# Optimization experiments

Measured on AMD Instinct MI355X. Metric: run time of the kernel, lower is better.

Reference implementation:

```python
import jax, jax.numpy as jnp
import numpy as np

C = 64

def setup_inputs() -> dict:
    key = jax.random.key(0)
    k1, k2, k3 = jax.random.split(key, 3)
    x = jax.random.normal(k1, (4, C, 64, 64), dtype=jnp.float32)
    # 1x1 conv weight/bias (kernel dims squeezed)
    W = jax.random.normal(k2, (C, C), dtype=jnp.float32) * (1.0 / np.sqrt(C))
    bconv = jax.random.normal(k3, (C,), dtype=jnp.float32) * 0.01
    return {"x": x, "W": W, "bconv": bconv}

def reference(x, W, bconv):
    b, c, h, w = x.shape
    hw = h * w
    # shared 1x1 conv: e = f = g (module applies the same conv three times)
    e = jnp.einsum('oc,bchw->bohw', W, x) + bconv[None, :, None, None]
    e = e.reshape(b, c, hw)
    # unscaled attention scores: (b, hw, hw)
    scores = jnp.einsum('bci,bcj->bij', e, e)
    attn = jax.nn.softmax(scores, axis=-1)
    # g @ attn: (b, c, hw)
    final = jnp.einsum('bci,bij->bcj', e, attn)
    return final.reshape(b, c, h, w) + x
```

## Files before the change

### kernel.cpp

```cpp
#include <hip/hip_runtime.h>
#include <math.h>

#define B 4
#define C 64
#define HW 4096

typedef _Float16 f16;
typedef f16 f16x8 __attribute__((ext_vector_type(8)));
typedef f16 f16x4 __attribute__((ext_vector_type(4)));
typedef f16 f16x2 __attribute__((ext_vector_type(2)));
typedef float f32x4 __attribute__((ext_vector_type(4)));
typedef float f32x16 __attribute__((ext_vector_type(16)));
typedef int i32x4 __attribute__((ext_vector_type(4)));
typedef f16x8 f16x8a __attribute__((aligned(8)));

#define MFMA16(a,b,c) __builtin_amdgcn_mfma_f32_16x16x32_f16(a,b,c,0,0,0)
#define MFMA32(a,b,c) __builtin_amdgcn_mfma_f32_32x32x16_f16(a,b,c,0,0,0)


__device__ __forceinline__ int swz_blk()     { int r = blockIdx.x; return (r & 7) * 32  + (r >> 3); }
__device__ __forceinline__ int swz_blk512()  { int r = blockIdx.x; return (r & 7) * 64  + (r >> 3); }
__device__ __forceinline__ int swz_blk2048() { int r = blockIdx.x; return (r & 7) * 256 + (r >> 3); }

__global__ __launch_bounds__(256) void k_e(
    const float* __restrict__ x, const float* __restrict__ W,
    const float* __restrict__ bconv, f16* __restrict__ et, f16* __restrict__ ec,
    float* __restrict__ mbuf)
{
  __shared__ float Ws[64][65];
  __shared__ float xs[64][64];
  __shared__ f16 es[64][72];
  __shared__ float msp[4][64];
  const int blk = swz_blk();
  const int b = blk >> 6;
  const int i0 = (blk & 63) * 64;
  const int tid = threadIdx.x;

  for (int k = tid; k < 64 * 64; k += 256) Ws[k >> 6][k & 63] = W[k];
  for (int k = tid; k < 64 * 64; k += 256)
    xs[k >> 6][k & 63] = x[((size_t)b * C + (k >> 6)) * HW + i0 + (k & 63)];
  __syncthreads();

  const int o = tid & 63;
  const int ig = tid >> 6;
  float acc[16];
  float bv = bconv[o];
  #pragma unroll
  for (int k = 0; k < 16; ++k) acc[k] = bv;
  for (int c = 0; c < C; ++c) {
    float wv = Ws[o][c];
    #pragma unroll
    for (int k = 0; k < 16; ++k) acc[k] = fmaf(wv, xs[c][ig * 16 + k], acc[k]);
  }
  #pragma unroll
  for (int k = 0; k < 16; ++k) {
    int ii = ig * 16 + k;
    f16 v = (f16)acc[k];
    et[((size_t)b * HW + i0 + ii) * C + o] = v;
    es[o][ii] = v;
  }
  __syncthreads();

  const int ii = tid & 63, og = tid >> 6;
  #pragma unroll
  for (int k = 0; k < 16; ++k) {
    int oo = og * 16 + k;
    ec[((size_t)b * C + oo) * HW + i0 + ii] = es[oo][ii];
  }

  {
    float s = 0.f;
    #pragma unroll
    for (int k = 0; k < 16; ++k) {
      float v = (float)es[og * 16 + k][ii];
      s = fmaf(v, v, s);
    }
    msp[og][ii] = s;
  }
  __syncthreads();
  if (tid < 64) {
    float mm = msp[0][tid] + msp[1][tid] + msp[2][tid] + msp[3][tid];
    mbuf[(size_t)b * HW + i0 + tid] = (float)(f16)mm;
  }
}

__global__ __launch_bounds__(256) __attribute__((amdgpu_waves_per_eu(4, 4)))
void k_stats(const f16* __restrict__ et, const float* __restrict__ mbuf,
             float* __restrict__ lpartial)
{
  __shared__ float lpart[4][36];
  const int blk = swz_blk2048();
  const int b  = blk >> 9;
  const int ib = (blk >> 2) & 127;
  const int jq = blk & 3;
  const int i0 = ib * 32;
  const int tid = threadIdx.x;
  const int wv = tid >> 6;
  const int lane = tid & 63;
  const int lr = lane & 15, lg = lane >> 4;
  const f16* etb = et + (size_t)b * HW * C;

  f16x8 a[2][2];
  #pragma unroll
  for (int is = 0; is < 2; ++is)
    #pragma unroll
    for (int kc = 0; kc < 2; ++kc)
      a[is][kc] = *(const f16x8*)(etb + (size_t)(i0 + is * 16 + lr) * C + kc * 32 + lg * 8);

  f32x4 ms4[2];
  #pragma unroll
  for (int is = 0; is < 2; ++is)
    ms4[is] = *(const f32x4*)(mbuf + (size_t)b * HW + i0 + is * 16 + lg * 4);

  float lacc[2][4] = {};
  for (int t = 0; t < 8; ++t) {
    const int j0 = jq * 1024 + (wv + 4 * t) * 32;
    #pragma unroll
    for (int js = 0; js < 2; ++js) {
      f16x8 b0 = *(const f16x8*)(etb + (size_t)(j0 + js * 16 + lr) * C + lg * 8);
      f16x8 b1 = *(const f16x8*)(etb + (size_t)(j0 + js * 16 + lr) * C + 32 + lg * 8);
      #pragma unroll
      for (int is = 0; is < 2; ++is) {
        f32x4 z = {0.f, 0.f, 0.f, 0.f};
        f32x4 S = MFMA16(a[is][0], b0, z);
        S = MFMA16(a[is][1], b1, S);
        #pragma unroll
        for (int r = 0; r < 4; ++r) lacc[is][r] += __expf(S[r] - ms4[is][r]);
      }
    }
  }

  #pragma unroll
  for (int m = 1; m < 16; m <<= 1)
    #pragma unroll
    for (int is = 0; is < 2; ++is)
      #pragma unroll
      for (int r = 0; r < 4; ++r) lacc[is][r] += __shfl_xor(lacc[is][r], m);

  if (lr == 0)
    #pragma unroll
    for (int is = 0; is < 2; ++is)
      #pragma unroll
      for (int r = 0; r < 4; ++r) lpart[wv][is * 16 + lg * 4 + r] = lacc[is][r];
  __syncthreads();

  if (tid < 32)
    lpartial[((size_t)b * HW + i0 + tid) * 4 + jq] =
        lpart[0][tid] + lpart[1][tid] + lpart[2][tid] + lpart[3][tid];
}

#define ETS 68
#define ECS 36
__global__ __launch_bounds__(512, 4) void k_out(
    const f16* __restrict__ et, const f16* __restrict__ ec,
    const float* __restrict__ mbuf, const float* __restrict__ lpartial,
    f16* __restrict__ partial)
{
  __shared__ __align__(16) f16 etL[2][32][ETS];
  __shared__ __align__(16) f16 ecL[2][64][ECS];
  __shared__ __align__(16) f16 maugAll[513][8];
  const int blk = swz_blk512();
  const int b  = blk >> 7;
  const int jb = (blk >> 3) & 15;
  const int iq = blk & 7;
  const int tid = threadIdx.x;
  const int w = tid >> 6;
  const int lane = tid & 63;
  const int l31 = lane & 31;
  const int h = lane >> 5;
  const int jbase = jb * 256 + w * 32;
  const int ibase = iq * 512;

  const f16* etb = et + (size_t)b * HW * C;
  const f16* ecb = ec + (size_t)b * C * HW;

  {
    float m = mbuf[(size_t)b * HW + ibase + tid];
    f32x4 lp = *(const f32x4*)&lpartial[((size_t)b * HW + ibase + tid) * 4];
    float l = lp[0] + lp[1] + lp[2] + lp[3];
    float d = __logf(l);
    f16 dh = (f16)d;
    f16 dl = (f16)(d - (float)dh);
    f16x8 row = {};
    row[0] = (f16)m; row[1] = dh; row[2] = dl;
    *(f16x8*)&maugAll[tid][0] = row;
    if (tid == 0) { f16x8 zz = {}; *(f16x8*)&maugAll[512][0] = zz; }
  }

  f16x8 baug = {};
  if (h == 0) { baug[0] = (f16)-1.f; baug[1] = (f16)-1.f; baug[2] = (f16)-1.f; }

  f16x8 bj[4];
  #pragma unroll
  for (int kc = 0; kc < 4; ++kc)
    bj[kc] = *(const f16x8*)(etb + (size_t)(jbase + l31) * C + kc * 16 + h * 8);

  f32x16 acc[2] = {};

  const bool se = (tid < 256);
  const int sei = tid >> 3;
  const int sec = (tid & 7) * 8;
  const int scc = (tid & 255) >> 2;
  const int sci = (tid & 3) * 8;

  if (se) *(f16x8a*)&etL[0][sei][sec] = *(const f16x8*)(etb + (size_t)(ibase + sei) * C + sec);
  else    *(f16x8a*)&ecL[0][scc][sci] = *(const f16x8*)(ecb + (size_t)scc * HW + ibase + sci);
  __syncthreads();

  for (int t = 0; t < 16; ++t) {
    const int cur = t & 1;
    const int i0c = ibase + t * 32;

    f16x8 sv;
    if (t < 15) {
      if (se) sv = *(const f16x8*)(etb + (size_t)(i0c + 32 + sei) * C + sec);
      else    sv = *(const f16x8*)(ecb + (size_t)scc * HW + (i0c + 32) + sci);
    }

    f16x8 bv[2][2];
    #pragma unroll
    for (int cs = 0; cs < 2; ++cs)
      #pragma unroll
      for (int kf = 0; kf < 2; ++kf)
        bv[cs][kf] = *(const f16x8a*)&ecL[cur][cs * 32 + l31][kf * 16 + h * 8];

    f16x8 af[4];
    #pragma unroll
    for (int kc = 0; kc < 4; ++kc)
      af[kc] = *(const f16x8a*)&etL[cur][l31][kc * 16 + h * 8];
    f16x8 aaug = *(const f16x8*)&maugAll[h ? 512 : (t * 32 + l31)][0];

    f32x16 z = {};
    f32x16 S = MFMA32(af[0], bj[0], z);
    S = MFMA32(af[1], bj[1], S);
    S = MFMA32(af[2], bj[2], S);
    S = MFMA32(af[3], bj[3], S);
    S = MFMA32(aaug, baug, S);

    float E[16];
    #pragma unroll
    for (int r = 0; r < 16; ++r) E[r] = __expf(S[r]);

    f16x8 pa[2];
    #pragma unroll
    for (int kf = 0; kf < 2; ++kf) {
      int A0 = __builtin_bit_cast(int, __builtin_amdgcn_cvt_pkrtz(E[kf * 8 + 0], E[kf * 8 + 1]));
      int A1 = __builtin_bit_cast(int, __builtin_amdgcn_cvt_pkrtz(E[kf * 8 + 2], E[kf * 8 + 3]));
      int B0 = __builtin_bit_cast(int, __builtin_amdgcn_cvt_pkrtz(E[kf * 8 + 4], E[kf * 8 + 5]));
      int B1 = __builtin_bit_cast(int, __builtin_amdgcn_cvt_pkrtz(E[kf * 8 + 6], E[kf * 8 + 7]));
      asm volatile("v_permlane32_swap_b32 %0, %1" : "+v"(A0), "+v"(B0));
      asm volatile("v_permlane32_swap_b32 %0, %1" : "+v"(A1), "+v"(B1));
      i32x4 fri = {A0, A1, B0, B1};
      pa[kf] = __builtin_bit_cast(f16x8, fri);
    }

    acc[0] = MFMA32(pa[0], bv[0][0], acc[0]);
    acc[1] = MFMA32(pa[0], bv[1][0], acc[1]);
    acc[0] = MFMA32(pa[1], bv[0][1], acc[0]);
    acc[1] = MFMA32(pa[1], bv[1][1], acc[1]);

    if (t < 15) {
      if (se) *(f16x8a*)&etL[cur ^ 1][sei][sec] = sv;
      else    *(f16x8a*)&ecL[cur ^ 1][scc][sci] = sv;
    }
    __syncthreads();
  }

  f16* pb = partial + (size_t)(iq * B + b) * HW * C;
  #pragma unroll
  for (int cs = 0; cs < 2; ++cs)
    #pragma unroll
    for (int r = 0; r < 16; ++r) {
      int j = jbase + (r & 3) + 8 * (r >> 2) + 4 * h;
      pb[(size_t)j * C + cs * 32 + l31] = (f16)acc[cs][r];
    }
}

__global__ __launch_bounds__(256) void k_reduce(
    const f16* __restrict__ partial, const float* __restrict__ x, float* __restrict__ out)
{
  __shared__ float tile[64][65];
  const int blk = swz_blk();
  const int b = blk >> 6;
  const int j0 = (blk & 63) * 64;
  const int tid = threadIdx.x;
  const int jj = tid >> 2, cq = (tid & 3) * 16;

  float a0[16] = {};
  for (int iq = 0; iq < 8; ++iq) {
    const f16* p = partial + ((size_t)(iq * B + b) * HW + j0 + jj) * C + cq;
    f16x8 v0 = *(const f16x8*)p;
    f16x8 v1 = *(const f16x8*)(p + 8);
    #pragma unroll
    for (int e = 0; e < 8; ++e) { a0[e] += (float)v0[e]; a0[8 + e] += (float)v1[e]; }
  }
  #pragma unroll
  for (int e = 0; e < 16; ++e) tile[jj][cq + e] = a0[e];
  __syncthreads();

  const int c = tid >> 2, jq = (tid & 3) * 16;
  #pragma unroll
  for (int k = 0; k < 4; ++k) {
    size_t idx = ((size_t)b * C + c) * HW + j0 + jq + k * 4;
    float4 xv = *(const float4*)(x + idx);
    float4 ov;
    ov.x = tile[jq + k * 4 + 0][c] + xv.x;
    ov.y = tile[jq + k * 4 + 1][c] + xv.y;
    ov.z = tile[jq + k * 4 + 2][c] + xv.z;
    ov.w = tile[jq + k * 4 + 3][c] + xv.w;
    *(float4*)(out + idx) = ov;
  }
}

extern "C" void kernel_launch(void* const* d_in, const int* in_sizes, int n_in,
                              void* d_out, int out_size, void* d_ws, size_t ws_size,
                              hipStream_t stream) {
  const float* x = (const float*)d_in[0];
  const float* W = (const float*)d_in[1];
  const float* bconv = (const float*)d_in[2];
  float* out = (float*)d_out;

  f16* et16 = (f16*)d_ws;
  f16* ec16 = et16 + (size_t)B * HW * C;
  float* mbuf = (float*)(ec16 + (size_t)B * HW * C);
  float* lpartial = mbuf + (size_t)B * HW;
  f16* partial = (f16*)(lpartial + (size_t)B * HW * 4);

  k_e<<<dim3(256), dim3(256), 0, stream>>>(x, W, bconv, et16, ec16, mbuf);
  k_stats<<<dim3(2048), dim3(256), 0, stream>>>(et16, mbuf, lpartial);
  k_out<<<dim3(512), dim3(512), 0, stream>>>(et16, ec16, mbuf, lpartial, partial);
  k_reduce<<<dim3(256), dim3(256), 0, stream>>>(partial, x, out);
}
```

Before: 74.09 us.

## Enlarge per-wave tiles in stats and output kernels, vectorize ec store

k_stats now has each block cover 64 query rows instead of 32, with half as many blocks, so every key fragment loaded is reused across four row sub-tiles. k_out drops to 256 threads per block, and each wave computes two 32-column j tiles, reusing the staged i-tile fragments from LDS twice. Each thread now stages both et and ec slices. k_e writes ec with 4-wide f16 vector stores instead of scalar stores. The goal is less global and LDS traffic per MFMA, paid for with more registers per wave and fewer waves per block.

```diff
diff --git a/kernel.cpp b/kernel.cpp
--- a/kernel.cpp
+++ b/kernel.cpp
@@ -8,7 +8,6 @@
 typedef _Float16 f16;
 typedef f16 f16x8 __attribute__((ext_vector_type(8)));
 typedef f16 f16x4 __attribute__((ext_vector_type(4)));
-typedef f16 f16x2 __attribute__((ext_vector_type(2)));
 typedef float f32x4 __attribute__((ext_vector_type(4)));
 typedef float f32x16 __attribute__((ext_vector_type(16)));
 typedef int i32x4 __attribute__((ext_vector_type(4)));
@@ -20,7 +19,7 @@
 
 __device__ __forceinline__ int swz_blk()     { int r = blockIdx.x; return (r & 7) * 32  + (r >> 3); }
 __device__ __forceinline__ int swz_blk512()  { int r = blockIdx.x; return (r & 7) * 64  + (r >> 3); }
-__device__ __forceinline__ int swz_blk2048() { int r = blockIdx.x; return (r & 7) * 256 + (r >> 3); }
+__device__ __forceinline__ int swz_blk1024() { int r = blockIdx.x; return (r & 7) * 128 + (r >> 3); }
 
 __global__ __launch_bounds__(256) void k_e(
     const float* __restrict__ x, const float* __restrict__ W,
@@ -29,7 +28,7 @@
 {
   __shared__ float Ws[64][65];
   __shared__ float xs[64][64];
-  __shared__ f16 es[64][72];
+  __shared__ __align__(16) f16 es[64][72];
   __shared__ float msp[4][64];
   const int blk = swz_blk();
   const int b = blk >> 6;
@@ -61,13 +60,18 @@
   }
   __syncthreads();
 
+  {
+    const int ii4 = (tid & 15) * 4;
+    const int ob = tid >> 4;
+    #pragma unroll
+    for (int k = 0; k < 4; ++k) {
+      int oo = ob + 16 * k;
+      f16x4 v = *(const f16x4*)&es[oo][ii4];
+      *(f16x4*)&ec[((size_t)b * C + oo) * HW + i0 + ii4] = v;
+    }
+  }
+
   const int ii = tid & 63, og = tid >> 6;
-  #pragma unroll
-  for (int k = 0; k < 16; ++k) {
-    int oo = og * 16 + k;
-    ec[((size_t)b * C + oo) * HW + i0 + ii] = es[oo][ii];
-  }
-
   {
     float s = 0.f;
     #pragma unroll
@@ -88,31 +92,31 @@
 void k_stats(const f16* __restrict__ et, const float* __restrict__ mbuf,
              float* __restrict__ lpartial)
 {
-  __shared__ float lpart[4][36];
-  const int blk = swz_blk2048();
-  const int b  = blk >> 9;
-  const int ib = (blk >> 2) & 127;
+  __shared__ float lpart[4][68];
+  const int blk = swz_blk1024();
+  const int b  = blk >> 8;
+  const int ib = (blk >> 2) & 63;
   const int jq = blk & 3;
-  const int i0 = ib * 32;
+  const int i0 = ib * 64;
   const int tid = threadIdx.x;
   const int wv = tid >> 6;
   const int lane = tid & 63;
   const int lr = lane & 15, lg = lane >> 4;
   const f16* etb = et + (size_t)b * HW * C;
 
-  f16x8 a[2][2];
-  #pragma unroll
-  for (int is = 0; is < 2; ++is)
+  f16x8 a[4][2];
+  #pragma unroll
+  for (int is = 0; is < 4; ++is)
     #pragma unroll
     for (int kc = 0; kc < 2; ++kc)
       a[is][kc] = *(const f16x8*)(etb + (size_t)(i0 + is * 16 + lr) * C + kc * 32 + lg * 8);
 
-  f32x4 ms4[2];
-  #pragma unroll
-  for (int is = 0; is < 2; ++is)
+  f32x4 ms4[4];
+  #pragma unroll
+  for (int is = 0; is < 4; ++is)
     ms4[is] = *(const f32x4*)(mbuf + (size_t)b * HW + i0 + is * 16 + lg * 4);
 
-  float lacc[2][4] = {};
+  float lacc[4][4] = {};
   for (int t = 0; t < 8; ++t) {
     const int j0 = jq * 1024 + (wv + 4 * t) * 32;
     #pragma unroll
@@ -120,7 +124,7 @@
       f16x8 b0 = *(const f16x8*)(etb + (size_t)(j0 + js * 16 + lr) * C + lg * 8);
       f16x8 b1 = *(const f16x8*)(etb + (size_t)(j0 + js * 16 + lr) * C + 32 + lg * 8);
       #pragma unroll
-      for (int is = 0; is < 2; ++is) {
+      for (int is = 0; is < 4; ++is) {
         f32x4 z = {0.f, 0.f, 0.f, 0.f};
         f32x4 S = MFMA16(a[is][0], b0, z);
         S = MFMA16(a[is][1], b1, S);
@@ -133,25 +137,26 @@
   #pragma unroll
   for (int m = 1; m < 16; m <<= 1)
     #pragma unroll
-    for (int is = 0; is < 2; ++is)
+    for (int is = 0; is < 4; ++is)
       #pragma unroll
       for (int r = 0; r < 4; ++r) lacc[is][r] += __shfl_xor(lacc[is][r], m);
 
   if (lr == 0)
     #pragma unroll
-    for (int is = 0; is < 2; ++is)
+    for (int is = 0; is < 4; ++is)
       #pragma unroll
       for (int r = 0; r < 4; ++r) lpart[wv][is * 16 + lg * 4 + r] = lacc[is][r];
   __syncthreads();
 
-  if (tid < 32)
+  if (tid < 64)
     lpartial[((size_t)b * HW + i0 + tid) * 4 + jq] =
         lpart[0][tid] + lpart[1][tid] + lpart[2][tid] + lpart[3][tid];
 }
 
 #define ETS 68
 #define ECS 36
-__global__ __launch_bounds__(512, 4) void k_out(
+__global__ __launch_bounds__(256) __attribute__((amdgpu_waves_per_eu(2, 4)))
+void k_out(
     const f16* __restrict__ et, const f16* __restrict__ ec,
     const float* __restrict__ mbuf, const float* __restrict__ lpartial,
     f16* __restrict__ partial)
@@ -168,53 +173,56 @@
   const int lane = tid & 63;
   const int l31 = lane & 31;
   const int h = lane >> 5;
-  const int jbase = jb * 256 + w * 32;
+  const int jbase = jb * 256 + w * 64;
   const int ibase = iq * 512;
 
   const f16* etb = et + (size_t)b * HW * C;
   const f16* ecb = ec + (size_t)b * C * HW;
 
-  {
-    float m = mbuf[(size_t)b * HW + ibase + tid];
-    f32x4 lp = *(const f32x4*)&lpartial[((size_t)b * HW + ibase + tid) * 4];
+  #pragma unroll
+  for (int rr = 0; rr < 2; ++rr) {
+    int i = tid + rr * 256;
+    float m = mbuf[(size_t)b * HW + ibase + i];
+    f32x4 lp = *(const f32x4*)&lpartial[((size_t)b * HW + ibase + i) * 4];
     float l = lp[0] + lp[1] + lp[2] + lp[3];
     float d = __logf(l);
     f16 dh = (f16)d;
     f16 dl = (f16)(d - (float)dh);
     f16x8 row = {};
     row[0] = (f16)m; row[1] = dh; row[2] = dl;
-    *(f16x8*)&maugAll[tid][0] = row;
-    if (tid == 0) { f16x8 zz = {}; *(f16x8*)&maugAll[512][0] = zz; }
-  }
+    *(f16x8*)&maugAll[i][0] = row;
+  }
+  if (tid == 0) { f16x8 zz = {}; *(f16x8*)&maugAll[512][0] = zz; }
 
   f16x8 baug = {};
   if (h == 0) { baug[0] = (f16)-1.f; baug[1] = (f16)-1.f; baug[2] = (f16)-1.f; }
 
-  f16x8 bj[4];
-  #pragma unroll
-  for (int kc = 0; kc < 4; ++kc)
-    bj[kc] = *(const f16x8*)(etb + (size_t)(jbase + l31) * C + kc * 16 + h * 8);
-
-  f32x16 acc[2] = {};
-
-  const bool se = (tid < 256);
+  f16x8 bj[2][4];
+  #pragma unroll
+  for (int jt = 0; jt < 2; ++jt)
+    #pragma unroll
+    for (int kc = 0; kc < 4; ++kc)
+      bj[jt][kc] = *(const f16x8*)(etb + (size_t)(jbase + jt * 32 + l31) * C + kc * 16 + h * 8);
+
+  f32x16 acc[2][2] = {};
+
   const int sei = tid >> 3;
   const int sec = (tid & 7) * 8;
-  const int scc = (tid & 255) >> 2;
+  const int scc = tid >> 2;
   const int sci = (tid & 3) * 8;
 
-  if (se) *(f16x8a*)&etL[0][sei][sec] = *(const f16x8*)(etb + (size_t)(ibase + sei) * C + sec);
-  else    *(f16x8a*)&ecL[0][scc][sci] = *(const f16x8*)(ecb + (size_t)scc * HW + ibase + sci);
+  *(f16x8a*)&etL[0][sei][sec] = *(const f16x8*)(etb + (size_t)(ibase + sei) * C + sec);
+  *(f16x8a*)&ecL[0][scc][sci] = *(const f16x8*)(ecb + (size_t)scc * HW + ibase + sci);
   __syncthreads();
 
   for (int t = 0; t < 16; ++t) {
     const int cur = t & 1;
     const int i0c = ibase + t * 32;
 
-    f16x8 sv;
+    f16x8 sve, svc;
     if (t < 15) {
-      if (se) sv = *(const f16x8*)(etb + (size_t)(i0c + 32 + sei) * C + sec);
-      else    sv = *(const f16x8*)(ecb + (size_t)scc * HW + (i0c + 32) + sci);
+      sve = *(const f16x8*)(etb + (size_t)(i0c + 32 + sei) * C + sec);
+      svc = *(const f16x8*)(ecb + (size_t)scc * HW + (i0c + 32) + sci);
     }
 
     f16x8 bv[2][2];
@@ -230,50 +238,51 @@
       af[kc] = *(const f16x8a*)&etL[cur][l31][kc * 16 + h * 8];
     f16x8 aaug = *(const f16x8*)&maugAll[h ? 512 : (t * 32 + l31)][0];
 
-    f32x16 z = {};
-    f32x16 S = MFMA32(af[0], bj[0], z);
-    S = MFMA32(af[1], bj[1], S);
-    S = MFMA32(af[2], bj[2], S);
-    S = MFMA32(af[3], bj[3], S);
-    S = MFMA32(aaug, baug, S);
-
-    float E[16];
-    #pragma unroll
-    for (int r = 0; r < 16; ++r) E[r] = __expf(S[r]);
-
-    f16x8 pa[2];
-    #pragma unroll
-    for (int kf = 0; kf < 2; ++kf) {
-      int A0 = __builtin_bit_cast(int, __builtin_amdgcn_cvt_pkrtz(E[kf * 8 + 0], E[kf * 8 + 1]));
-      int A1 = __builtin_bit_cast(int, __builtin_amdgcn_cvt_pkrtz(E[kf * 8 + 2], E[kf * 8 + 3]));
-      int B0 = __builtin_bit_cast(int, __builtin_amdgcn_cvt_pkrtz(E[kf * 8 + 4], E[kf * 8 + 5]));
-      int B1 = __builtin_bit_cast(int, __builtin_amdgcn_cvt_pkrtz(E[kf * 8 + 6], E[kf * 8 + 7]));
-      asm volatile("v_permlane32_swap_b32 %0, %1" : "+v"(A0), "+v"(B0));
-      asm volatile("v_permlane32_swap_b32 %0, %1" : "+v"(A1), "+v"(B1));
-      i32x4 fri = {A0, A1, B0, B1};
-      pa[kf] = __builtin_bit_cast(f16x8, fri);
-    }
-
-    acc[0] = MFMA32(pa[0], bv[0][0], acc[0]);
-    acc[1] = MFMA32(pa[0], bv[1][0], acc[1]);
-    acc[0] = MFMA32(pa[1], bv[0][1], acc[0]);
-    acc[1] = MFMA32(pa[1], bv[1][1], acc[1]);
+    #pragma unroll
+    for (int jt = 0; jt < 2; ++jt) {
+      f32x16 z = {};
+      f32x16 S = MFMA32(af[0], bj[jt][0], z);
+      S = MFMA32(af[1], bj[jt][1], S);
+      S = MFMA32(af[2], bj[jt][2], S);
+      S = MFMA32(af[3], bj[jt][3], S);
+      S = MFMA32(aaug, baug, S);
+
+      f16x8 pa[2];
+      #pragma unroll
+      for (int kf = 0; kf < 2; ++kf) {
+        int A0 = __builtin_bit_cast(int, __builtin_amdgcn_cvt_pkrtz(__expf(S[kf * 8 + 0]), __expf(S[kf * 8 + 1])));
+        int A1 = __builtin_bit_cast(int, __builtin_amdgcn_cvt_pkrtz(__expf(S[kf * 8 + 2]), __expf(S[kf * 8 + 3])));
+        int B0 = __builtin_bit_cast(int, __builtin_amdgcn_cvt_pkrtz(__expf(S[kf * 8 + 4]), __expf(S[kf * 8 + 5])));
+        int B1 = __builtin_bit_cast(int, __builtin_amdgcn_cvt_pkrtz(__expf(S[kf * 8 + 6]), __expf(S[kf * 8 + 7])));
+        asm volatile("v_permlane32_swap_b32 %0, %1" : "+v"(A0), "+v"(B0));
+        asm volatile("v_permlane32_swap_b32 %0, %1" : "+v"(A1), "+v"(B1));
+        i32x4 fri = {A0, A1, B0, B1};
+        pa[kf] = __builtin_bit_cast(f16x8, fri);
+      }
+
+      acc[jt][0] = MFMA32(pa[0], bv[0][0], acc[jt][0]);
+      acc[jt][1] = MFMA32(pa[0], bv[1][0], acc[jt][1]);
+      acc[jt][0] = MFMA32(pa[1], bv[0][1], acc[jt][0]);
+      acc[jt][1] = MFMA32(pa[1], bv[1][1], acc[jt][1]);
+    }
 
     if (t < 15) {
-      if (se) *(f16x8a*)&etL[cur ^ 1][sei][sec] = sv;
-      else    *(f16x8a*)&ecL[cur ^ 1][scc][sci] = sv;
+      *(f16x8a*)&etL[cur ^ 1][sei][sec] = sve;
+      *(f16x8a*)&ecL[cur ^ 1][scc][sci] = svc;
     }
     __syncthreads();
   }
 
   f16* pb = partial + (size_t)(iq * B + b) * HW * C;
   #pragma unroll
-  for (int cs = 0; cs < 2; ++cs)
-    #pragma unroll
-    for (int r = 0; r < 16; ++r) {
-      int j = jbase + (r & 3) + 8 * (r >> 2) + 4 * h;
-      pb[(size_t)j * C + cs * 32 + l31] = (f16)acc[cs][r];
-    }
+  for (int jt = 0; jt < 2; ++jt)
+    #pragma unroll
+    for (int cs = 0; cs < 2; ++cs)
+      #pragma unroll
+      for (int r = 0; r < 16; ++r) {
+        int j = jbase + jt * 32 + (r & 3) + 8 * (r >> 2) + 4 * h;
+        pb[(size_t)j * C + cs * 32 + l31] = (f16)acc[jt][cs][r];
+      }
 }
 
 __global__ __launch_bounds__(256) void k_reduce(
@@ -327,7 +336,7 @@
   f16* partial = (f16*)(lpartial + (size_t)B * HW * 4);
 
   k_e<<<dim3(256), dim3(256), 0, stream>>>(x, W, bconv, et16, ec16, mbuf);
-  k_stats<<<dim3(2048), dim3(256), 0, stream>>>(et16, mbuf, lpartial);
-  k_out<<<dim3(512), dim3(512), 0, stream>>>(et16, ec16, mbuf, lpartial, partial);
+  k_stats<<<dim3(1024), dim3(256), 0, stream>>>(et16, mbuf, lpartial);
+  k_out<<<dim3(512), dim3(256), 0, stream>>>(et16, ec16, mbuf, lpartial, partial);
   k_reduce<<<dim3(256), dim3(256), 0, stream>>>(partial, x, out);
 }
```

After: 90.41 us. +22.0%, slower.
